# Kernel tuning notes

Measured on AMD Instinct MI355X. Metric: run time of the kernel, lower is better.

Reference implementation:

```python
import jax, jax.numpy as jnp
import numpy as np

D_MODEL = 768
NUM_HEADS = 8
DEPTH = D_MODEL // NUM_HEADS


def setup_inputs() -> dict:
    key = jax.random.key(0)
    ks = jax.random.split(key, 12)
    B, S = 4, 2048
    s = 0.02
    return {
        "q_in": jax.random.normal(ks[0], (B, S, D_MODEL), jnp.float32),
        "k_in": jax.random.normal(ks[1], (B, S, D_MODEL), jnp.float32),
        "v_in": jax.random.normal(ks[2], (B, S, D_MODEL), jnp.float32),
        "mask": jnp.zeros((B, 1, 1, S), jnp.float32),
        "wq": jax.random.normal(ks[3], (D_MODEL, D_MODEL), jnp.float32) * s,
        "bq": jax.random.normal(ks[4], (D_MODEL,), jnp.float32) * s,
        "wk": jax.random.normal(ks[5], (D_MODEL, D_MODEL), jnp.float32) * s,
        "bk": jax.random.normal(ks[6], (D_MODEL,), jnp.float32) * s,
        "wv": jax.random.normal(ks[7], (D_MODEL, D_MODEL), jnp.float32) * s,
        "bv": jax.random.normal(ks[8], (D_MODEL,), jnp.float32) * s,
        "wo": jax.random.normal(ks[9], (D_MODEL, D_MODEL), jnp.float32) * s,
        "bo": jax.random.normal(ks[10], (D_MODEL,), jnp.float32) * s,
    }


def _split_heads(x, B):
    # [B, S, D] -> [B, H, S, depth]
    return x.reshape(B, -1, NUM_HEADS, DEPTH).transpose(0, 2, 1, 3)


def reference(q_in, k_in, v_in, mask, wq, bq, wk, bk, wv, bv, wo, bo):
    B = q_in.shape[0]
    q = _split_heads(q_in @ wq + bq, B)   # [B,H,Sq,d]
    k = _split_heads(k_in @ wk + bk, B)   # [B,H,Sk,d]
    v = _split_heads(v_in @ wv + bv, B)   # [B,H,Sk,d]

    scale = 1.0 / jnp.sqrt(jnp.float32(DEPTH))
    logits = jnp.einsum("bhqd,bhkd->bhqk", q, k) * scale
    logits = logits + mask * (-1e9)
    attn = jax.nn.softmax(logits, axis=-1)            # [B,H,Sq,Sk]
    ctx = jnp.einsum("bhqk,bhkd->bhqd", attn, v)
    ctx = ctx.transpose(0, 2, 1, 3).reshape(B, -1, D_MODEL)  # concat heads
    out = ctx @ wo + bo
    return out, attn
```

## Files before the change

kernel.cpp:

```cpp
#include <hip/hip_runtime.h>
#include <hip/hip_bf16.h>
#include <stdint.h>


#define SEQ 2048
#define DM 768
#define NB 4
#define NH 8
#define DEP 96
#define MROWS 8192

typedef __bf16 bf16x8 __attribute__((ext_vector_type(8)));
typedef float f32x4 __attribute__((ext_vector_type(4)));

__device__ inline unsigned short f2b(float f) {
    return __builtin_bit_cast(unsigned short, (__bf16)f);
}
__device__ inline bf16x8 ld_frag(const unsigned short* p) {
    return __builtin_bit_cast(bf16x8, *(const uint4*)p);
}

__global__ __launch_bounds__(256) void wt_kernel(
    const float* __restrict__ w0, const float* __restrict__ w1,
    const float* __restrict__ w2, const float* __restrict__ w3,
    unsigned short* __restrict__ wt)
{
    __shared__ float tile[32][33];
    int mat = blockIdx.z;
    const float* w = mat == 0 ? w0 : mat == 1 ? w1 : mat == 2 ? w2 : w3;
    unsigned short* dst = wt + (size_t)mat * DM * DM;
    int k0 = blockIdx.x * 32, n0 = blockIdx.y * 32;
    int tx = threadIdx.x & 31, ty = threadIdx.x >> 5;
#pragma unroll
    for (int i = 0; i < 4; i++)
        tile[ty + i * 8][tx] = w[(size_t)(k0 + ty + i * 8) * DM + n0 + tx];
    __syncthreads();
#pragma unroll
    for (int i = 0; i < 4; i++)
        dst[(size_t)(n0 + ty + i * 8) * DM + k0 + tx] = f2b(tile[tx][ty + i * 8]);
}

__global__ __launch_bounds__(256) void proj_kernel(
    const float* __restrict__ qin, const float* __restrict__ kin, const float* __restrict__ vin,
    const unsigned short* __restrict__ wt,
    const float* __restrict__ bq, const float* __restrict__ bk, const float* __restrict__ bv,
    unsigned short* __restrict__ qb, unsigned short* __restrict__ kb, unsigned short* __restrict__ vb)
{
    __shared__ unsigned short As[128 * 32];
    __shared__ unsigned short Bs[128 * 32];

    int z = blockIdx.z;
    const float* x = z == 0 ? qin : z == 1 ? kin : vin;
    const unsigned short* W = wt + (size_t)z * DM * DM;
    const float* bias = z == 0 ? bq : z == 1 ? bk : bv;
    unsigned short* out = z == 0 ? qb : z == 1 ? kb : vb;

    int tid = threadIdx.x;
    int lane = tid & 63, wv_ = tid >> 6;
    int col = lane & 15, quad = lane >> 4;
    int m0 = blockIdx.x * 128, n0 = blockIdx.y * 128;
    int mi = (wv_ & 1) * 64, ni = (wv_ >> 1) * 64;
    int srow = tid >> 1, shalf = (tid & 1) * 16;

    f32x4 acc[4][4] = {};
    for (int kk = 0; kk < DM; kk += 32) {
        __syncthreads();
        {
            const float* xa = x + (size_t)(m0 + srow) * DM + kk + shalf;
            float4 f0 = *(const float4*)xa;
            float4 f1 = *(const float4*)(xa + 4);
            float4 f2 = *(const float4*)(xa + 8);
            float4 f3 = *(const float4*)(xa + 12);
            bf16x8 p0, p1;
            p0[0] = (__bf16)f0.x; p0[1] = (__bf16)f0.y; p0[2] = (__bf16)f0.z; p0[3] = (__bf16)f0.w;
            p0[4] = (__bf16)f1.x; p0[5] = (__bf16)f1.y; p0[6] = (__bf16)f1.z; p0[7] = (__bf16)f1.w;
            p1[0] = (__bf16)f2.x; p1[1] = (__bf16)f2.y; p1[2] = (__bf16)f2.z; p1[3] = (__bf16)f2.w;
            p1[4] = (__bf16)f3.x; p1[5] = (__bf16)f3.y; p1[6] = (__bf16)f3.z; p1[7] = (__bf16)f3.w;
            *(uint4*)&As[srow * 32 + shalf]     = __builtin_bit_cast(uint4, p0);
            *(uint4*)&As[srow * 32 + shalf + 8] = __builtin_bit_cast(uint4, p1);
        }
        {
            const unsigned short* wb = W + (size_t)(n0 + srow) * DM + kk + shalf;
            *(uint4*)&Bs[srow * 32 + shalf]     = *(const uint4*)wb;
            *(uint4*)&Bs[srow * 32 + shalf + 8] = *(const uint4*)(wb + 8);
        }
        __syncthreads();
        bf16x8 af[4], bfr[4];
#pragma unroll
        for (int mt = 0; mt < 4; mt++)
            af[mt] = ld_frag(&As[(mi + mt * 16 + col) * 32 + quad * 8]);
#pragma unroll
        for (int nt = 0; nt < 4; nt++)
            bfr[nt] = ld_frag(&Bs[(ni + nt * 16 + col) * 32 + quad * 8]);
#pragma unroll
        for (int mt = 0; mt < 4; mt++)
#pragma unroll
            for (int nt = 0; nt < 4; nt++)
                acc[mt][nt] = __builtin_amdgcn_mfma_f32_16x16x32_bf16(af[mt], bfr[nt], acc[mt][nt], 0, 0, 0);
    }
#pragma unroll
    for (int mt = 0; mt < 4; mt++) {
        int grow_base = m0 + mi + mt * 16 + quad * 4;
#pragma unroll
        for (int nt = 0; nt < 4; nt++) {
            int gcol = n0 + ni + nt * 16 + col;
            float bv_ = bias[gcol];
            int h = gcol / DEP, d = gcol % DEP;
#pragma unroll
            for (int r = 0; r < 4; r++) {
                int grow = grow_base + r;
                int b = grow >> 11, s = grow & 2047;
                out[((size_t)((b * NH + h) * SEQ + s)) * DEP + d] = f2b(acc[mt][nt][r] + bv_);
            }
        }
    }
}

__global__ __launch_bounds__(256) void vt_kernel(
    const unsigned short* __restrict__ vb, unsigned short* __restrict__ vt)
{
    __shared__ unsigned short tile[32][33];
    int bh = blockIdx.z;
    int s0 = blockIdx.x * 32, d0 = blockIdx.y * 32;
    int tx = threadIdx.x & 31, ty = threadIdx.x >> 5;
    const unsigned short* src = vb + (size_t)bh * SEQ * DEP;
    unsigned short* dst = vt + (size_t)bh * DEP * SEQ;
#pragma unroll
    for (int i = 0; i < 4; i++)
        tile[ty + i * 8][tx] = src[(size_t)(s0 + ty + i * 8) * DEP + d0 + tx];
    __syncthreads();
#pragma unroll
    for (int i = 0; i < 4; i++)
        dst[(size_t)(d0 + ty + i * 8) * SEQ + s0 + tx] = tile[tx][ty + i * 8];
}

__global__ __launch_bounds__(256, 4) void attn_kernel(
    const unsigned short* __restrict__ qb, const unsigned short* __restrict__ kb,
    const unsigned short* __restrict__ vt, const float* __restrict__ mask,
    float* __restrict__ attn_out, unsigned short* __restrict__ ctx)
{
    __shared__ float mask_s[SEQ];
    __shared__ unsigned short p_lds[4][16 * 72];

    int tid = threadIdx.x;
    int w = tid >> 6, lane = tid & 63, col = lane & 15, quad = lane >> 4;
    int bh = blockIdx.y;
    int b = bh >> 3, h = bh & 7;
    int q0 = blockIdx.x * 64 + w * 16;

    const unsigned short* Qp = qb + (size_t)bh * SEQ * DEP;
    const unsigned short* Kp = kb + (size_t)bh * SEQ * DEP;
    const unsigned short* Vp = vt + (size_t)bh * DEP * SEQ;
    float* attn = attn_out + (size_t)bh * SEQ * SEQ;

    for (int i = tid; i < SEQ; i += 256)
        mask_s[i] = mask[b * SEQ + i] * (-1e9f);
    __syncthreads();

    bf16x8 aq[3];
#pragma unroll
    for (int ks = 0; ks < 3; ks++)
        aq[ks] = ld_frag(Qp + (size_t)(q0 + col) * DEP + ks * 32 + quad * 8);

    const float scale = 0.10206207261596575f;
    float lsum[4] = {0.f, 0.f, 0.f, 0.f};

    for (int kt = 0; kt < SEQ; kt += 64) {
#pragma unroll
        for (int nt = 0; nt < 4; nt++) {
            const unsigned short* kr = Kp + (size_t)(kt + nt * 16 + col) * DEP;
            f32x4 c = {0.f, 0.f, 0.f, 0.f};
#pragma unroll
            for (int ks = 0; ks < 3; ks++)
                c = __builtin_amdgcn_mfma_f32_16x16x32_bf16(aq[ks], ld_frag(kr + ks * 32 + quad * 8), c, 0, 0, 0);
            float mv = mask_s[kt + nt * 16 + col];
#pragma unroll
            for (int r = 0; r < 4; r++)
                lsum[r] += __expf(c[r] * scale + mv);
        }
    }
#pragma unroll
    for (int r = 0; r < 4; r++) {
        float v = lsum[r];
        v += __shfl_xor(v, 1); v += __shfl_xor(v, 2);
        v += __shfl_xor(v, 4); v += __shfl_xor(v, 8);
        lsum[r] = 1.0f / v;
    }

    f32x4 o[6] = {};
    for (int kt = 0; kt < SEQ; kt += 64) {
#pragma unroll
        for (int nt = 0; nt < 4; nt++) {
            const unsigned short* kr = Kp + (size_t)(kt + nt * 16 + col) * DEP;
            f32x4 c = {0.f, 0.f, 0.f, 0.f};
#pragma unroll
            for (int ks = 0; ks < 3; ks++)
                c = __builtin_amdgcn_mfma_f32_16x16x32_bf16(aq[ks], ld_frag(kr + ks * 32 + quad * 8), c, 0, 0, 0);
            float mv = mask_s[kt + nt * 16 + col];
#pragma unroll
            for (int r = 0; r < 4; r++) {
                float p = __expf(c[r] * scale + mv) * lsum[r];
                attn[(size_t)(q0 + quad * 4 + r) * SEQ + kt + nt * 16 + col] = p;
                p_lds[w][(quad * 4 + r) * 72 + nt * 16 + col] = f2b(p);
            }
        }
        bf16x8 pa0 = ld_frag(&p_lds[w][col * 72 + quad * 8]);
        bf16x8 pa1 = ld_frag(&p_lds[w][col * 72 + 32 + quad * 8]);
        const unsigned short* vbase = Vp + (size_t)col * SEQ + kt;
#pragma unroll
        for (int dt = 0; dt < 6; dt++) {
            const unsigned short* vr = vbase + (size_t)dt * 16 * SEQ;
            o[dt] = __builtin_amdgcn_mfma_f32_16x16x32_bf16(pa0, ld_frag(vr + quad * 8), o[dt], 0, 0, 0);
            o[dt] = __builtin_amdgcn_mfma_f32_16x16x32_bf16(pa1, ld_frag(vr + 32 + quad * 8), o[dt], 0, 0, 0);
        }
    }
#pragma unroll
    for (int dt = 0; dt < 6; dt++)
#pragma unroll
        for (int r = 0; r < 4; r++) {
            int qrow = q0 + quad * 4 + r;
            ctx[(size_t)(b * SEQ + qrow) * DM + h * DEP + dt * 16 + col] = f2b(o[dt][r]);
        }
}

__global__ __launch_bounds__(256) void oproj_kernel(
    const unsigned short* __restrict__ ctx, const unsigned short* __restrict__ woT,
    const float* __restrict__ bo, float* __restrict__ out)
{
    __shared__ unsigned short As[128 * 32];
    __shared__ unsigned short Bs[128 * 32];

    int tid = threadIdx.x;
    int lane = tid & 63, wv_ = tid >> 6;
    int col = lane & 15, quad = lane >> 4;
    int m0 = blockIdx.x * 128, n0 = blockIdx.y * 128;
    int mi = (wv_ & 1) * 64, ni = (wv_ >> 1) * 64;
    int srow = tid >> 1, shalf = (tid & 1) * 16;

    f32x4 acc[4][4] = {};
    for (int kk = 0; kk < DM; kk += 32) {
        __syncthreads();
        {
            const unsigned short* xa = ctx + (size_t)(m0 + srow) * DM + kk + shalf;
            *(uint4*)&As[srow * 32 + shalf]     = *(const uint4*)xa;
            *(uint4*)&As[srow * 32 + shalf + 8] = *(const uint4*)(xa + 8);
            const unsigned short* wb = woT + (size_t)(n0 + srow) * DM + kk + shalf;
            *(uint4*)&Bs[srow * 32 + shalf]     = *(const uint4*)wb;
            *(uint4*)&Bs[srow * 32 + shalf + 8] = *(const uint4*)(wb + 8);
        }
        __syncthreads();
        bf16x8 af[4], bfr[4];
#pragma unroll
        for (int mt = 0; mt < 4; mt++)
            af[mt] = ld_frag(&As[(mi + mt * 16 + col) * 32 + quad * 8]);
#pragma unroll
        for (int nt = 0; nt < 4; nt++)
            bfr[nt] = ld_frag(&Bs[(ni + nt * 16 + col) * 32 + quad * 8]);
#pragma unroll
        for (int mt = 0; mt < 4; mt++)
#pragma unroll
            for (int nt = 0; nt < 4; nt++)
                acc[mt][nt] = __builtin_amdgcn_mfma_f32_16x16x32_bf16(af[mt], bfr[nt], acc[mt][nt], 0, 0, 0);
    }
#pragma unroll
    for (int mt = 0; mt < 4; mt++) {
        int grow_base = m0 + mi + mt * 16 + quad * 4;
#pragma unroll
        for (int nt = 0; nt < 4; nt++) {
            int gcol = n0 + ni + nt * 16 + col;
            float bv_ = bo[gcol];
#pragma unroll
            for (int r = 0; r < 4; r++)
                out[(size_t)(grow_base + r) * DM + gcol] = acc[mt][nt][r] + bv_;
        }
    }
}

extern "C" void kernel_launch(void* const* d_in, const int* in_sizes, int n_in,
                              void* d_out, int out_size, void* d_ws, size_t ws_size,
                              hipStream_t stream) {
    (void)in_sizes; (void)n_in; (void)out_size; (void)ws_size;
    const float* q_in = (const float*)d_in[0];
    const float* k_in = (const float*)d_in[1];
    const float* v_in = (const float*)d_in[2];
    const float* mask = (const float*)d_in[3];
    const float* wq = (const float*)d_in[4];
    const float* bq = (const float*)d_in[5];
    const float* wk = (const float*)d_in[6];
    const float* bk = (const float*)d_in[7];
    const float* wv = (const float*)d_in[8];
    const float* bv = (const float*)d_in[9];
    const float* wo = (const float*)d_in[10];
    const float* bo = (const float*)d_in[11];

    unsigned short* ws = (unsigned short*)d_ws;
    const size_t WMAT = (size_t)DM * DM;
    const size_t QKV = (size_t)NB * NH * SEQ * DEP;
    unsigned short* wT    = ws;
    unsigned short* qbuf  = ws + 4 * WMAT;
    unsigned short* kbuf  = qbuf + QKV;
    unsigned short* vbuf  = kbuf + QKV;
    unsigned short* vtbuf = vbuf + QKV;
    unsigned short* ctxbuf = vtbuf + QKV;

    float* out_f = (float*)d_out;
    float* attn_f = out_f + (size_t)NB * SEQ * DM;

    dim3 blk(256);
    wt_kernel<<<dim3(24, 24, 4), blk, 0, stream>>>(wq, wk, wv, wo, wT);
    proj_kernel<<<dim3(MROWS / 128, DM / 128, 3), blk, 0, stream>>>(
        q_in, k_in, v_in, wT, bq, bk, bv, qbuf, kbuf, vbuf);
    vt_kernel<<<dim3(SEQ / 32, DEP / 32, NB * NH), blk, 0, stream>>>(vbuf, vtbuf);
    attn_kernel<<<dim3(SEQ / 64, NB * NH), blk, 0, stream>>>(
        qbuf, kbuf, vtbuf, mask, attn_f, ctxbuf);
    oproj_kernel<<<dim3(MROWS / 128, DM / 128), blk, 0, stream>>>(
        ctxbuf, wT + 3 * WMAT, bo, out_f);
}
```

Baseline: 1.083 ms.

## Split attention over key halves, prepack inputs to bf16, use direct global-to-LDS loads

The attention kernel now gives each block 32 query rows and splits the key range between two wave pairs. Partial softmax sums and context accumulators are combined through shared memory, which doubles the grid and raises the occupancy hint to 8. A new pre-pass converts the fp32 q/k/v inputs to bf16 so the projection GEMM can stream tiles with global_load_lds instead of going through registers, and the output projection uses the same loads. This adds an extra conversion kernel and memory traffic, reuses the bf16 input buffer for the V transpose, and adds extra barriers in the attention epilogue.

```diff
diff --git a/kernel.cpp b/kernel.cpp
--- a/kernel.cpp
+++ b/kernel.cpp
@@ -19,6 +19,11 @@
 __device__ inline bf16x8 ld_frag(const unsigned short* p) {
     return __builtin_bit_cast(bf16x8, *(const uint4*)p);
 }
+__device__ inline void gload_lds16(const unsigned short* g, unsigned short* l) {
+    __builtin_amdgcn_global_load_lds(
+        (const __attribute__((address_space(1))) unsigned int*)g,
+        (__attribute__((address_space(3))) unsigned int*)l, 16, 0, 0);
+}
 
 __global__ __launch_bounds__(256) void wt_kernel(
     const float* __restrict__ w0, const float* __restrict__ w1,
@@ -40,9 +45,24 @@
         dst[(size_t)(n0 + ty + i * 8) * DM + k0 + tx] = f2b(tile[tx][ty + i * 8]);
 }
 
+__global__ __launch_bounds__(256) void xcvt_kernel(
+    const float* __restrict__ q, const float* __restrict__ k, const float* __restrict__ v,
+    unsigned short* __restrict__ xb)
+{
+    int z = blockIdx.z;
+    const float* src = z == 0 ? q : z == 1 ? k : v;
+    unsigned short* dst = xb + (size_t)z * MROWS * DM;
+    size_t i = ((size_t)blockIdx.x * 256 + threadIdx.x) * 8;
+    float4 f0 = *(const float4*)(src + i);
+    float4 f1 = *(const float4*)(src + i + 4);
+    bf16x8 p;
+    p[0] = (__bf16)f0.x; p[1] = (__bf16)f0.y; p[2] = (__bf16)f0.z; p[3] = (__bf16)f0.w;
+    p[4] = (__bf16)f1.x; p[5] = (__bf16)f1.y; p[6] = (__bf16)f1.z; p[7] = (__bf16)f1.w;
+    *(uint4*)(dst + i) = __builtin_bit_cast(uint4, p);
+}
+
 __global__ __launch_bounds__(256) void proj_kernel(
-    const float* __restrict__ qin, const float* __restrict__ kin, const float* __restrict__ vin,
-    const unsigned short* __restrict__ wt,
+    const unsigned short* __restrict__ xb, const unsigned short* __restrict__ wt,
     const float* __restrict__ bq, const float* __restrict__ bk, const float* __restrict__ bv,
     unsigned short* __restrict__ qb, unsigned short* __restrict__ kb, unsigned short* __restrict__ vb)
 {
@@ -50,7 +70,7 @@
     __shared__ unsigned short Bs[128 * 32];
 
     int z = blockIdx.z;
-    const float* x = z == 0 ? qin : z == 1 ? kin : vin;
+    const unsigned short* x = xb + (size_t)z * MROWS * DM;
     const unsigned short* W = wt + (size_t)z * DM * DM;
     const float* bias = z == 0 ? bq : z == 1 ? bk : bv;
     unsigned short* out = z == 0 ? qb : z == 1 ? kb : vb;
@@ -60,30 +80,15 @@
     int col = lane & 15, quad = lane >> 4;
     int m0 = blockIdx.x * 128, n0 = blockIdx.y * 128;
     int mi = (wv_ & 1) * 64, ni = (wv_ >> 1) * 64;
-    int srow = tid >> 1, shalf = (tid & 1) * 16;
+    int sr = tid >> 2, so = (tid & 3) * 8;
 
     f32x4 acc[4][4] = {};
     for (int kk = 0; kk < DM; kk += 32) {
         __syncthreads();
-        {
-            const float* xa = x + (size_t)(m0 + srow) * DM + kk + shalf;
-            float4 f0 = *(const float4*)xa;
-            float4 f1 = *(const float4*)(xa + 4);
-            float4 f2 = *(const float4*)(xa + 8);
-            float4 f3 = *(const float4*)(xa + 12);
-            bf16x8 p0, p1;
-            p0[0] = (__bf16)f0.x; p0[1] = (__bf16)f0.y; p0[2] = (__bf16)f0.z; p0[3] = (__bf16)f0.w;
-            p0[4] = (__bf16)f1.x; p0[5] = (__bf16)f1.y; p0[6] = (__bf16)f1.z; p0[7] = (__bf16)f1.w;
-            p1[0] = (__bf16)f2.x; p1[1] = (__bf16)f2.y; p1[2] = (__bf16)f2.z; p1[3] = (__bf16)f2.w;
-            p1[4] = (__bf16)f3.x; p1[5] = (__bf16)f3.y; p1[6] = (__bf16)f3.z; p1[7] = (__bf16)f3.w;
-            *(uint4*)&As[srow * 32 + shalf]     = __builtin_bit_cast(uint4, p0);
-            *(uint4*)&As[srow * 32 + shalf + 8] = __builtin_bit_cast(uint4, p1);
-        }
-        {
-            const unsigned short* wb = W + (size_t)(n0 + srow) * DM + kk + shalf;
-            *(uint4*)&Bs[srow * 32 + shalf]     = *(const uint4*)wb;
-            *(uint4*)&Bs[srow * 32 + shalf + 8] = *(const uint4*)(wb + 8);
-        }
+        gload_lds16(x + (size_t)(m0 + sr) * DM + kk + so,      &As[tid * 8]);
+        gload_lds16(x + (size_t)(m0 + 64 + sr) * DM + kk + so, &As[2048 + tid * 8]);
+        gload_lds16(W + (size_t)(n0 + sr) * DM + kk + so,      &Bs[tid * 8]);
+        gload_lds16(W + (size_t)(n0 + 64 + sr) * DM + kk + so, &Bs[2048 + tid * 8]);
         __syncthreads();
         bf16x8 af[4], bfr[4];
 #pragma unroll
@@ -134,19 +139,23 @@
         dst[(size_t)(d0 + ty + i * 8) * SEQ + s0 + tx] = tile[tx][ty + i * 8];
 }
 
-__global__ __launch_bounds__(256, 4) void attn_kernel(
+__global__ __launch_bounds__(256, 8) void attn_kernel(
     const unsigned short* __restrict__ qb, const unsigned short* __restrict__ kb,
     const unsigned short* __restrict__ vt, const float* __restrict__ mask,
     float* __restrict__ attn_out, unsigned short* __restrict__ ctx)
 {
     __shared__ float mask_s[SEQ];
     __shared__ unsigned short p_lds[4][16 * 72];
+    __shared__ float lsum_x[2][2][16];
+    __shared__ f32x4 o_xchg[2][64];
 
     int tid = threadIdx.x;
     int w = tid >> 6, lane = tid & 63, col = lane & 15, quad = lane >> 4;
+    int qg = w & 1, kh = w >> 1;
     int bh = blockIdx.y;
     int b = bh >> 3, h = bh & 7;
-    int q0 = blockIdx.x * 64 + w * 16;
+    int q0 = blockIdx.x * 32 + qg * 16;
+    int kbeg = kh * (SEQ / 2), kend = kbeg + SEQ / 2;
 
     const unsigned short* Qp = qb + (size_t)bh * SEQ * DEP;
     const unsigned short* Kp = kb + (size_t)bh * SEQ * DEP;
@@ -165,7 +174,7 @@
     const float scale = 0.10206207261596575f;
     float lsum[4] = {0.f, 0.f, 0.f, 0.f};
 
-    for (int kt = 0; kt < SEQ; kt += 64) {
+    for (int kt = kbeg; kt < kend; kt += 64) {
 #pragma unroll
         for (int nt = 0; nt < 4; nt++) {
             const unsigned short* kr = Kp + (size_t)(kt + nt * 16 + col) * DEP;
@@ -184,11 +193,20 @@
         float v = lsum[r];
         v += __shfl_xor(v, 1); v += __shfl_xor(v, 2);
         v += __shfl_xor(v, 4); v += __shfl_xor(v, 8);
-        lsum[r] = 1.0f / v;
-    }
+        lsum[r] = v;
+    }
+    if (col == 0) {
+#pragma unroll
+        for (int r = 0; r < 4; r++)
+            lsum_x[qg][kh][quad * 4 + r] = lsum[r];
+    }
+    __syncthreads();
+#pragma unroll
+    for (int r = 0; r < 4; r++)
+        lsum[r] = 1.0f / (lsum_x[qg][0][quad * 4 + r] + lsum_x[qg][1][quad * 4 + r]);
 
     f32x4 o[6] = {};
-    for (int kt = 0; kt < SEQ; kt += 64) {
+    for (int kt = kbeg; kt < kend; kt += 64) {
 #pragma unroll
         for (int nt = 0; nt < 4; nt++) {
             const unsigned short* kr = Kp + (size_t)(kt + nt * 16 + col) * DEP;
@@ -214,13 +232,23 @@
             o[dt] = __builtin_amdgcn_mfma_f32_16x16x32_bf16(pa1, ld_frag(vr + 32 + quad * 8), o[dt], 0, 0, 0);
         }
     }
-#pragma unroll
-    for (int dt = 0; dt < 6; dt++)
-#pragma unroll
-        for (int r = 0; r < 4; r++) {
-            int qrow = q0 + quad * 4 + r;
-            ctx[(size_t)(b * SEQ + qrow) * DM + h * DEP + dt * 16 + col] = f2b(o[dt][r]);
-        }
+
+#pragma unroll
+    for (int dt = 0; dt < 6; dt++) {
+        __syncthreads();
+        if (kh == 1) o_xchg[qg][lane] = o[dt];
+        __syncthreads();
+        if (kh == 0) o[dt] += o_xchg[qg][lane];
+    }
+    if (kh == 0) {
+#pragma unroll
+        for (int dt = 0; dt < 6; dt++)
+#pragma unroll
+            for (int r = 0; r < 4; r++) {
+                int qrow = q0 + quad * 4 + r;
+                ctx[(size_t)(b * SEQ + qrow) * DM + h * DEP + dt * 16 + col] = f2b(o[dt][r]);
+            }
+    }
 }
 
 __global__ __launch_bounds__(256) void oproj_kernel(
@@ -235,19 +263,15 @@
     int col = lane & 15, quad = lane >> 4;
     int m0 = blockIdx.x * 128, n0 = blockIdx.y * 128;
     int mi = (wv_ & 1) * 64, ni = (wv_ >> 1) * 64;
-    int srow = tid >> 1, shalf = (tid & 1) * 16;
+    int sr = tid >> 2, so = (tid & 3) * 8;
 
     f32x4 acc[4][4] = {};
     for (int kk = 0; kk < DM; kk += 32) {
         __syncthreads();
-        {
-            const unsigned short* xa = ctx + (size_t)(m0 + srow) * DM + kk + shalf;
-            *(uint4*)&As[srow * 32 + shalf]     = *(const uint4*)xa;
-            *(uint4*)&As[srow * 32 + shalf + 8] = *(const uint4*)(xa + 8);
-            const unsigned short* wb = woT + (size_t)(n0 + srow) * DM + kk + shalf;
-            *(uint4*)&Bs[srow * 32 + shalf]     = *(const uint4*)wb;
-            *(uint4*)&Bs[srow * 32 + shalf + 8] = *(const uint4*)(wb + 8);
-        }
+        gload_lds16(ctx + (size_t)(m0 + sr) * DM + kk + so,      &As[tid * 8]);
+        gload_lds16(ctx + (size_t)(m0 + 64 + sr) * DM + kk + so, &As[2048 + tid * 8]);
+        gload_lds16(woT + (size_t)(n0 + sr) * DM + kk + so,      &Bs[tid * 8]);
+        gload_lds16(woT + (size_t)(n0 + 64 + sr) * DM + kk + so, &Bs[2048 + tid * 8]);
         __syncthreads();
         bf16x8 af[4], bfr[4];
 #pragma unroll
@@ -300,18 +324,20 @@
     unsigned short* qbuf  = ws + 4 * WMAT;
     unsigned short* kbuf  = qbuf + QKV;
     unsigned short* vbuf  = kbuf + QKV;
-    unsigned short* vtbuf = vbuf + QKV;
-    unsigned short* ctxbuf = vtbuf + QKV;
+    unsigned short* xb    = vbuf + QKV;
+    unsigned short* vtbuf = xb;
+    unsigned short* ctxbuf = xb + QKV;
 
     float* out_f = (float*)d_out;
     float* attn_f = out_f + (size_t)NB * SEQ * DM;
 
     dim3 blk(256);
     wt_kernel<<<dim3(24, 24, 4), blk, 0, stream>>>(wq, wk, wv, wo, wT);
+    xcvt_kernel<<<dim3(3072, 1, 3), blk, 0, stream>>>(q_in, k_in, v_in, xb);
     proj_kernel<<<dim3(MROWS / 128, DM / 128, 3), blk, 0, stream>>>(
-        q_in, k_in, v_in, wT, bq, bk, bv, qbuf, kbuf, vbuf);
+        xb, wT, bq, bk, bv, qbuf, kbuf, vbuf);
     vt_kernel<<<dim3(SEQ / 32, DEP / 32, NB * NH), blk, 0, stream>>>(vbuf, vtbuf);
-    attn_kernel<<<dim3(SEQ / 64, NB * NH), blk, 0, stream>>>(
+    attn_kernel<<<dim3(SEQ / 32, NB * NH), blk, 0, stream>>>(
         qbuf, kbuf, vtbuf, mask, attn_f, ctxbuf);
     oproj_kernel<<<dim3(MROWS / 128, DM / 128), blk, 0, stream>>>(
         ctxbuf, wT + 3 * WMAT, bo, out_f);
```

Measured after the change: 1.330 ms. 1.23x slower.
